# Kernel tuning notes

Measured on AMD Instinct MI355X. Metric: run time of the kernel, lower is better.

Reference implementation:

```python
import jax, jax.numpy as jnp
import numpy as np

NODES_PER_GRAPH = 40
NEG_SLOPE = 0.1


def gcn_conv(x, src, dst, deg_inv_sqrt, W, b):
    # PyG GCNConv: h = x @ W.T; symmetric-normalized aggregation with self-loops; + bias
    h = x @ W.T                                   # [N, out]
    norm = deg_inv_sqrt[src] * deg_inv_sqrt[dst]  # [E]
    msgs = h[src] * norm[:, None]                 # [E, out]
    agg = jax.ops.segment_sum(msgs, dst, num_segments=x.shape[0])
    # self-loop contribution: norm_ii = deg_inv_sqrt[i]^2 = 1/deg[i]
    agg = agg + h * (deg_inv_sqrt ** 2)[:, None]
    return agg + b


def setup_inputs() -> dict:
    key = jax.random.key(0)
    ks = jax.random.split(key, 12)
    N, E, C = 200000, 1000000, 40
    hid1, hid2, hid3, lin1, lin2, out = 128, 256, 128, 512, 128, 1

    def glorot(k, shape):
        fan_in = shape[-1]
        return jax.random.normal(k, shape, dtype=jnp.float32) * (1.0 / np.sqrt(fan_in))

    x = jax.random.normal(ks[0], (N, C), dtype=jnp.float32)
    edge_index = jax.random.randint(ks[1], (2, E), 0, N, dtype=jnp.int64)
    return {
        "x": x,
        "edge_index": edge_index,
        "W1": glorot(ks[2], (hid1, C)), "b1": jnp.zeros((hid1,), jnp.float32),
        "W2": glorot(ks[3], (hid2, hid1)), "b2": jnp.zeros((hid2,), jnp.float32),
        "W3": glorot(ks[4], (hid3, hid2)), "b3": jnp.zeros((hid3,), jnp.float32),
        "L1w": glorot(ks[5], (lin1, NODES_PER_GRAPH * hid3)), "L1b": jnp.zeros((lin1,), jnp.float32),
        "L2w": glorot(ks[6], (lin2, lin1)), "L2b": jnp.zeros((lin2,), jnp.float32),
        "L3w": glorot(ks[7], (out, lin2)), "L3b": jnp.zeros((out,), jnp.float32),
    }


def reference(x, edge_index, W1, b1, W2, b2, W3, b3, L1w, L1b, L2w, L2b, L3w, L3b):
    N = x.shape[0]
    src, dst = edge_index[0], edge_index[1]
    # degree with self-loops (edge weight 1), shared by all three convs
    deg = jax.ops.segment_sum(jnp.ones_like(dst, dtype=x.dtype), dst, num_segments=N) + 1.0
    deg_inv_sqrt = jax.lax.rsqrt(deg)

    lrelu = lambda v: jax.nn.leaky_relu(v, NEG_SLOPE)

    h = lrelu(gcn_conv(x, src, dst, deg_inv_sqrt, W1, b1))
    # dropout is identity in eval mode
    h = lrelu(gcn_conv(h, src, dst, deg_inv_sqrt, W2, b2))
    h = lrelu(gcn_conv(h, src, dst, deg_inv_sqrt, W3, b3))

    g = h.reshape(N // NODES_PER_GRAPH, -1)   # [G, 40*hid3]
    g = lrelu(g @ L1w.T + L1b)
    g = lrelu(g @ L2w.T + L2b)
    g = g @ L3w.T + L3b
    return jax.nn.sigmoid(g)                   # [G, 1]
```

## Files before the change

kernel.cpp:

```cpp
#include <hip/hip_runtime.h>
#include <cmath>

#define CDIV(a,b) (((a)+(b)-1)/(b))

typedef unsigned short bf16_t;
using short8 = __attribute__((ext_vector_type(8))) short;
using f32x4  = __attribute__((ext_vector_type(4))) float;
using u16x4  = __attribute__((ext_vector_type(4))) unsigned short;
using u16x8  = __attribute__((ext_vector_type(8))) unsigned short;

__device__ __forceinline__ float bf2f(unsigned short b) {
    unsigned u = ((unsigned)b) << 16;
    float f;
    __builtin_memcpy(&f, &u, 4);
    return f;
}
__device__ __forceinline__ unsigned short f2bf(float f) {
    unsigned u;
    __builtin_memcpy(&u, &f, 4);
    u = (u + 0x7FFFu + ((u >> 16) & 1u)) >> 16;
    return (unsigned short)u;
}

__device__ __forceinline__ void gload16(const bf16_t* g, unsigned short* l) {
    __builtin_amdgcn_global_load_lds(
        (const __attribute__((address_space(1))) void*)(g),
        (__attribute__((address_space(3))) void*)(l), 16, 0, 0);
}

__device__ __forceinline__ int edge_src(const int* ei, int E, int f, int i) {
    return f ? ei[2 * (size_t)i] : ei[i];
}
__device__ __forceinline__ int edge_dst(const int* ei, int E, int f, int i) {
    return f ? ei[2 * ((size_t)E + (size_t)i)] : ei[(size_t)E + (size_t)i];
}

__global__ __launch_bounds__(256) void k_packhist(const int* __restrict__ ei, int E,
                                                  int* __restrict__ src32,
                                                  int* __restrict__ dst32,
                                                  int* __restrict__ cnt8, int N) {
    __shared__ int sflag;
    int t = threadIdx.x;
    if (t < 64) {
        unsigned v = (unsigned)ei[2 * t + 1];
        unsigned long long m = __ballot(v != 0u);
        if (t == 0) sflag = (m == 0ULL) ? 1 : 0;
    }
    __syncthreads();
    int i = blockIdx.x * 256 + t;
    if (i >= E) return;
    int f = sflag;
    int s = edge_src(ei, E, f, i);
    int d = edge_dst(ei, E, f, i);
    src32[i] = s;
    dst32[i] = d;
    if ((unsigned)d < (unsigned)N)
        atomicAdd(&cnt8[(blockIdx.x & 7) * N + d], 1);
}

__global__ void k_blockred(const int* __restrict__ cnt8, int* __restrict__ bsum, int N) {
    __shared__ int sd[256];
    int b = blockIdx.x, t = threadIdx.x;
    int base = b * 1024 + t * 4;
    int s = 0;
#pragma unroll
    for (int i = 0; i < 4; i++) {
        int idx = base + i;
        if (idx < N)
#pragma unroll
            for (int r = 0; r < 8; r++) s += cnt8[r * N + idx];
    }
    sd[t] = s; __syncthreads();
    for (int off = 128; off > 0; off >>= 1) { if (t < off) sd[t] += sd[t + off]; __syncthreads(); }
    if (t == 0) bsum[b] = sd[0];
}

__global__ void k_scanwrite(const int* __restrict__ cnt8, const int* __restrict__ bsum,
                            int* __restrict__ rowptr, int* __restrict__ cur,
                            float* __restrict__ dis, int N, int nb) {
    __shared__ int sb[256];
    __shared__ int sd[256];
    int b = blockIdx.x, t = threadIdx.x;
    int v0 = (t < nb) ? bsum[t] : 0;
    sb[t] = v0; __syncthreads();
    for (int off = 1; off < 256; off <<= 1) {
        int y = (t >= off) ? sb[t - off] : 0;
        __syncthreads();
        sb[t] += y;
        __syncthreads();
    }
    int block_pre = (b == 0) ? 0 : sb[b - 1];

    int base = b * 1024 + t * 4;
    int tot[4]; int s = 0;
#pragma unroll
    for (int i = 0; i < 4; i++) {
        int idx = base + i;
        tot[i] = 0;
        if (idx < N) {
#pragma unroll
            for (int r = 0; r < 8; r++) tot[i] += cnt8[r * N + idx];
        }
        s += tot[i];
    }
    sd[t] = s; __syncthreads();
    for (int off = 1; off < 256; off <<= 1) {
        int y = (t >= off) ? sd[t - off] : 0;
        __syncthreads();
        sd[t] += y;
        __syncthreads();
    }
    int pre = block_pre + sd[t] - s;
#pragma unroll
    for (int i = 0; i < 4; i++) {
        int idx = base + i;
        if (idx < N) {
            rowptr[idx] = pre;
            cur[idx] = pre;
            dis[idx] = rsqrtf((float)tot[i] + 1.0f);
            pre += tot[i];
        } else if (idx == N) {
            rowptr[N] = pre;
        }
    }
}

#define FILL_EPB 4096
__global__ __launch_bounds__(256) void k_fill_r(
        const int* __restrict__ src32, const int* __restrict__ dst32, int E,
        int* __restrict__ cur, int* __restrict__ csr, int N, int NR) {
    int r = blockIdx.x & 7;
    int chunk = blockIdx.x >> 3;
    int lo = r * NR;
    int hi = min(lo + NR, N);
    int base = chunk * FILL_EPB;
    int end = min(base + FILL_EPB, E);
    for (int i = base + threadIdx.x; i < end; i += 256) {
        int d = dst32[i];
        if (d >= lo && d < hi) {
            int s = src32[i];
            if ((unsigned)s < (unsigned)N) {
                int p = atomicAdd(&cur[d], 1);
                csr[p] = s;
            }
        }
    }
}


struct WcSeg { const float* src; bf16_t* dst; int M, KW, KP, nchunk; };

__global__ __launch_bounds__(256) void k_wconv(WcSeg s0, WcSeg s1, WcSeg s2,
                                               WcSeg s3, WcSeg s4, WcSeg s5,
                                               int wtotal, int* __restrict__ zdst,
                                               int total) {
    int i = blockIdx.x * 256 + threadIdx.x;
    if (i >= total) return;
    if (i >= wtotal) {
        int4 z = {0, 0, 0, 0};
        *(int4*)(zdst + (size_t)(i - wtotal) * 4) = z;
        return;
    }
    WcSeg s;
    if (i < s0.nchunk) s = s0;
    else if ((i -= s0.nchunk) < s1.nchunk) s = s1;
    else if ((i -= s1.nchunk) < s2.nchunk) s = s2;
    else if ((i -= s2.nchunk) < s3.nchunk) s = s3;
    else if ((i -= s3.nchunk) < s4.nchunk) s = s4;
    else { i -= s4.nchunk; s = s5; }
    int cpr = s.KP >> 3;
    int row = i / cpr, kk = (i % cpr) << 3;
    short8 v = {};
    if (kk < s.KW) {
        const float4* p = (const float4*)(s.src + (size_t)row * s.KW + kk);
        float4 a = p[0], b = p[1];
        v[0] = (short)f2bf(a.x); v[1] = (short)f2bf(a.y);
        v[2] = (short)f2bf(a.z); v[3] = (short)f2bf(a.w);
        v[4] = (short)f2bf(b.x); v[5] = (short)f2bf(b.y);
        v[6] = (short)f2bf(b.z); v[7] = (short)f2bf(b.w);
    }
    *(short8*)(s.dst + (size_t)row * s.KP + kk) = v;
}


template <bool CBF, bool BIAS, int ACT, bool SPLIT>
__global__ __launch_bounds__(256) void gemm_mfma(
        const bf16_t* __restrict__ A, const bf16_t* __restrict__ Wb,
        const float* __restrict__ bias, void* __restrict__ Cv,
        int N, int K, int M, int Kseg, int nx, int ny) {
    constexpr int BM = 128, BK = 64;
    __shared__ __align__(16) unsigned short lds[4 * 64 * 68];
    unsigned short* Als = lds;
    unsigned short* Bls = lds + BM * BK;

    int t = threadIdx.x;
    int lane = t & 63, wid = t >> 6;
    int quad = lane >> 4, l15 = lane & 15;
    int wave_m = wid & 1, wave_n = wid >> 1;

    int bx, by, bz;
    if (SPLIT) {
        int bid = (int)blockIdx.x;
        int xcd = bid & 7, li = bid >> 3;
        bx = li % nx;
        int pl = li / nx;
        int ppx = (int)(gridDim.x >> 3) / nx;
        int pair = xcd * ppx + pl;
        by = pair % ny;
        bz = pair / ny;
    } else {
        bx = blockIdx.x; by = blockIdx.y; bz = 0;
    }

    int bm0 = by * BM;
    int bn0 = bx * BM;
    int kbeg = SPLIT ? bz * Kseg : 0;
    int kend = SPLIT ? min(kbeg + Kseg, K) : K;

    f32x4 acc[4][4] = {};

    for (int k0 = kbeg; k0 < kend; k0 += BK) {
#pragma unroll
        for (int it = 0; it < 4; it++) {
            int idx = t + it * 256;
            int row = idx >> 3, sc = idx & 7;
            int c = sc ^ (row & 7);
            int ga = bm0 + row; if (ga >= N) ga = N - 1;
            gload16(A + (size_t)ga * K + k0 + c * 8, Als + idx * 8);
            gload16(Wb + (size_t)(bn0 + row) * K + k0 + c * 8, Bls + idx * 8);
        }
        __syncthreads();

#pragma unroll
        for (int ks = 0; ks < 2; ks++) {
            short8 af[4], bfr[4];
            int ck = ks * 4 + quad;
            int sw = (ck ^ (l15 & 7)) << 3;
#pragma unroll
            for (int mt = 0; mt < 4; mt++)
                af[mt] = *(const short8*)&Als[(wave_m * 64 + mt * 16 + l15) * BK + sw];
#pragma unroll
            for (int nt = 0; nt < 4; nt++)
                bfr[nt] = *(const short8*)&Bls[(wave_n * 64 + nt * 16 + l15) * BK + sw];
#pragma unroll
            for (int mt = 0; mt < 4; mt++)
#pragma unroll
                for (int nt = 0; nt < 4; nt++)
                    acc[mt][nt] = __builtin_amdgcn_mfma_f32_16x16x32_bf16(
                        af[mt], bfr[nt], acc[mt][nt], 0, 0, 0);
        }
        __syncthreads();
    }

    if (!SPLIT && CBF) {
        constexpr int TST = 68;
        unsigned short* tw = lds + wid * 64 * TST;
#pragma unroll
        for (int mt = 0; mt < 4; mt++) {
#pragma unroll
            for (int nt = 0; nt < 4; nt++) {
                int tcol = nt * 16 + l15;
                float bv = BIAS ? bias[bn0 + wave_n * 64 + tcol] : 0.f;
#pragma unroll
                for (int r = 0; r < 4; r++) {
                    float x = acc[mt][nt][r];
                    if (BIAS) x += bv;
                    if (ACT == 1) x = x > 0.f ? x : 0.1f * x;
                    tw[(mt * 16 + quad * 4 + r) * TST + tcol] = f2bf(x);
                }
            }
        }
        __syncthreads();
        bf16_t* C = (bf16_t*)Cv;
        int lrow0 = lane >> 3, lcol = (lane & 7) * 8;
#pragma unroll
        for (int it = 0; it < 8; it++) {
            int lrow = it * 8 + lrow0;
            int row = bm0 + wave_m * 64 + lrow;
            if (row < N) {
                u16x8 v = *(const u16x8*)&tw[lrow * TST + lcol];
                *(u16x8*)&C[(size_t)row * M + bn0 + wave_n * 64 + lcol] = v;
            }
        }
    } else {
        float* Pz = SPLIT ? ((float*)Cv + (size_t)bz * N * M) : (float*)Cv;
#pragma unroll
        for (int mt = 0; mt < 4; mt++) {
            int rbase = bm0 + wave_m * 64 + mt * 16 + quad * 4;
#pragma unroll
            for (int nt = 0; nt < 4; nt++) {
                int col = bn0 + wave_n * 64 + nt * 16 + l15;
                float bv = (BIAS && !SPLIT) ? bias[col] : 0.f;
#pragma unroll
                for (int r = 0; r < 4; r++) {
                    int row = rbase + r;
                    if (row >= N) continue;
                    float x = acc[mt][nt][r];
                    if (!SPLIT) {
                        if (BIAS) x += bv;
                        if (ACT == 1) x = x > 0.f ? x : 0.1f * x;
                    }
                    Pz[(size_t)row * M + col] = x;
                }
            }
        }
    }
}

__global__ __launch_bounds__(256) void gemm_mlp2(
        const float* __restrict__ part6,
        const float* __restrict__ L1b,
        const bf16_t* __restrict__ Wb,
        float* __restrict__ Pout,
        int G) {
    constexpr int BM = 128, BK = 64, K = 512, M = 128, NY = 40;
    __shared__ __align__(16) unsigned short lds[2 * BM * BK];
    unsigned short* Als = lds;
    unsigned short* Bls = lds + BM * BK;

    int t = threadIdx.x;
    int lane = t & 63, wid = t >> 6;
    int quad = lane >> 4, l15 = lane & 15;
    int wave_m = wid & 1, wave_n = wid >> 1;

    int bid = (int)blockIdx.x;
    int xcd = bid & 7, li = bid >> 3;
    int ppx = (int)(gridDim.x >> 3);
    int pair = xcd * ppx + li;
    int by = pair % NY;
    int bz = pair / NY;

    int bm0 = by * BM;
    int kbeg = bz * (K / 4);
    size_t GK = (size_t)G * K;

    f32x4 acc[4][4] = {};

    for (int k0 = kbeg; k0 < kbeg + K / 4; k0 += BK) {
#pragma unroll
        for (int it = 0; it < 4; it++) {
            int idx = t + it * 256;
            int row = idx >> 3, sc = idx & 7;
            int cW = sc ^ (row & 7);
            gload16(Wb + (size_t)row * K + k0 + cW * 8, Bls + idx * 8);
            int g = bm0 + row; if (g >= G) g = G - 1;
            const float* pb = part6 + (size_t)g * K + k0 + sc * 8;
            float v[8] = {};
#pragma unroll
            for (int z = 0; z < 6; z++) {
                const float* pz = pb + (size_t)z * GK;
                float4 a = *(const float4*)pz;
                float4 b = *(const float4*)(pz + 4);
                v[0] += a.x; v[1] += a.y; v[2] += a.z; v[3] += a.w;
                v[4] += b.x; v[5] += b.y; v[6] += b.z; v[7] += b.w;
            }
            float4 b0 = *(const float4*)&L1b[k0 + sc * 8];
            float4 b1 = *(const float4*)&L1b[k0 + sc * 8 + 4];
            float bb[8] = {b0.x, b0.y, b0.z, b0.w, b1.x, b1.y, b1.z, b1.w};
            u16x8 o;
#pragma unroll
            for (int j = 0; j < 8; j++) {
                float xv = v[j] + bb[j];
                xv = xv > 0.f ? xv : 0.1f * xv;
                o[j] = f2bf(xv);
            }
            *(u16x8*)&Als[row * BK + ((sc ^ (row & 7)) << 3)] = o;
        }
        __syncthreads();

#pragma unroll
        for (int ks = 0; ks < 2; ks++) {
            short8 af[4], bfr[4];
            int ck = ks * 4 + quad;
            int sw = (ck ^ (l15 & 7)) << 3;
#pragma unroll
            for (int mt = 0; mt < 4; mt++)
                af[mt] = *(const short8*)&Als[(wave_m * 64 + mt * 16 + l15) * BK + sw];
#pragma unroll
            for (int nt = 0; nt < 4; nt++)
                bfr[nt] = *(const short8*)&Bls[(wave_n * 64 + nt * 16 + l15) * BK + sw];
#pragma unroll
            for (int mt = 0; mt < 4; mt++)
#pragma unroll
                for (int nt = 0; nt < 4; nt++)
                    acc[mt][nt] = __builtin_amdgcn_mfma_f32_16x16x32_bf16(
                        af[mt], bfr[nt], acc[mt][nt], 0, 0, 0);
        }
        __syncthreads();
    }

    float* Pz = Pout + (size_t)bz * G * M;
#pragma unroll
    for (int mt = 0; mt < 4; mt++) {
        int rbase = bm0 + wave_m * 64 + mt * 16 + quad * 4;
#pragma unroll
        for (int nt = 0; nt < 4; nt++) {
            int col = wave_n * 64 + nt * 16 + l15;
#pragma unroll
            for (int r = 0; r < 4; r++) {
                int row = rbase + r;
                if (row >= G) continue;
                Pz[(size_t)row * M + col] = acc[mt][nt][r];
            }
        }
    }
}

__global__ __launch_bounds__(256, 3) void gemm_fused23(
        const bf16_t* __restrict__ A,
        const bf16_t* __restrict__ W2,
        const float*  __restrict__ b2,
        const bf16_t* __restrict__ W3,
        bf16_t* __restrict__ C,
        int N) {
    __shared__ __align__(16) unsigned short lds[24576];
    unsigned short* Als  = lds;
    unsigned short* Bls  = lds + 4096;
    unsigned short* H2ls = lds;
    unsigned short* B2ls = lds + 16384;

    int t = threadIdx.x;
    int lane = t & 63, wid = t >> 6;
    int quad = lane >> 4, l15 = lane & 15;
    int wm = wid & 1, wn = wid >> 1;
    int bm0 = blockIdx.x * 64;

    float bv[8];
#pragma unroll
    for (int nt = 0; nt < 8; nt++) bv[nt] = b2[wn * 128 + nt * 16 + l15];

    f32x4 acc1[2][8] = {};
    for (int k0 = 0; k0 < 128; k0 += 64) {
#pragma unroll
        for (int it = 0; it < 2; it++) {
            int idx = t + it * 256;
            int row = idx >> 3, sc = idx & 7;
            int c = sc ^ (row & 7);
            int g = bm0 + row; if (g >= N) g = N - 1;
            gload16(A + (size_t)g * 128 + k0 + c * 8, Als + idx * 8);
        }
#pragma unroll
        for (int it = 0; it < 8; it++) {
            int idx = t + it * 256;
            int row = idx >> 3, sc = idx & 7;
            int c = sc ^ (row & 7);
            gload16(W2 + (size_t)row * 128 + k0 + c * 8, Bls + idx * 8);
        }
        __syncthreads();
#pragma unroll
        for (int ks = 0; ks < 2; ks++) {
            int ck = ks * 4 + quad;
            int sw = (ck ^ (l15 & 7)) << 3;
            short8 af[2];
#pragma unroll
            for (int mt = 0; mt < 2; mt++)
                af[mt] = *(const short8*)&Als[(wm * 32 + mt * 16 + l15) * 64 + sw];
#pragma unroll
            for (int nt = 0; nt < 8; nt++) {
                short8 bfr = *(const short8*)&Bls[(wn * 128 + nt * 16 + l15) * 64 + sw];
#pragma unroll
                for (int mt = 0; mt < 2; mt++)
                    acc1[mt][nt] = __builtin_amdgcn_mfma_f32_16x16x32_bf16(
                        af[mt], bfr, acc1[mt][nt], 0, 0, 0);
            }
        }
        __syncthreads();
    }

#pragma unroll
    for (int it = 0; it < 4; it++) {
        int idx = t + it * 256;
        int row = idx >> 3, sc = idx & 7;
        int c = sc ^ (row & 7);
        gload16(W3 + (size_t)row * 256 + c * 8, B2ls + idx * 8);
    }

#pragma unroll
    for (int mt = 0; mt < 2; mt++) {
#pragma unroll
        for (int nt = 0; nt < 8; nt++) {
            int col = wn * 128 + nt * 16 + l15;
            int chunk = col >> 3, within = col & 7;
#pragma unroll
            for (int r = 0; r < 4; r++) {
                int row = wm * 32 + mt * 16 + quad * 4 + r;
                float xv = acc1[mt][nt][r] + bv[nt];
                xv = xv > 0.f ? xv : 0.1f * xv;
                H2ls[row * 256 + ((chunk ^ (row & 7)) << 3) + within] = f2bf(xv);
            }
        }
    }
    __syncthreads();

    f32x4 acc2[2][4] = {};
    for (int k0 = 0; k0 < 256; k0 += 64) {
        if (k0 > 0) {
#pragma unroll
            for (int it = 0; it < 4; it++) {
                int idx = t + it * 256;
                int row = idx >> 3, sc = idx & 7;
                int c = sc ^ (row & 7);
                gload16(W3 + (size_t)row * 256 + k0 + c * 8, B2ls + idx * 8);
            }
            __syncthreads();
        }
#pragma unroll
        for (int ks = 0; ks < 2; ks++) {
            int kc = (k0 >> 3) + ks * 4 + quad;
            int swa = (kc ^ (l15 & 7)) << 3;
            int swb = ((ks * 4 + quad) ^ (l15 & 7)) << 3;
            short8 af[2], bfr[4];
#pragma unroll
            for (int mt = 0; mt < 2; mt++)
                af[mt] = *(const short8*)&H2ls[(wm * 32 + mt * 16 + l15) * 256 + swa];
#pragma unroll
            for (int nt = 0; nt < 4; nt++)
                bfr[nt] = *(const short8*)&B2ls[(wn * 64 + nt * 16 + l15) * 64 + swb];
#pragma unroll
            for (int mt = 0; mt < 2; mt++)
#pragma unroll
                for (int nt = 0; nt < 4; nt++)
                    acc2[mt][nt] = __builtin_amdgcn_mfma_f32_16x16x32_bf16(
                        af[mt], bfr[nt], acc2[mt][nt], 0, 0, 0);
        }
        __syncthreads();
    }

    constexpr int TST = 68;
    unsigned short* tw = lds + wid * 32 * TST;
#pragma unroll
    for (int mt = 0; mt < 2; mt++) {
#pragma unroll
        for (int nt = 0; nt < 4; nt++) {
            int tcol = nt * 16 + l15;
#pragma unroll
            for (int r = 0; r < 4; r++)
                tw[(mt * 16 + quad * 4 + r) * TST + tcol] = f2bf(acc2[mt][nt][r]);
        }
    }
    __syncthreads();
    int lrow0 = lane >> 3, lcol = (lane & 7) * 8;
#pragma unroll
    for (int it = 0; it < 4; it++) {
        int lrow = it * 8 + lrow0;
        int row = bm0 + wm * 32 + lrow;
        if (row < N) {
            u16x8 v = *(const u16x8*)&tw[lrow * TST + lcol];
            *(u16x8*)&C[(size_t)row * 128 + wn * 64 + lcol] = v;
        }
    }
}


template <int F, bool BACT>
__global__ __launch_bounds__(256) void k_agg(
        const bf16_t* __restrict__ H, const int* __restrict__ rowptr,
        const int* __restrict__ csr, const float* __restrict__ dis,
        const float* __restrict__ bias, bf16_t* __restrict__ out, int N) {
    constexpr int SUB = F / 8;
    constexpr int NPW = 64 / SUB;
    constexpr int SH  = (SUB == 16) ? 4 : 3;
    int gtid = blockIdx.x * 256 + threadIdx.x;
    int wave = gtid >> 6, lane = gtid & 63;
    int sub = lane >> SH, sl = lane & (SUB - 1);
    int node = wave * NPW + sub;
    if (node >= N) return;
    float di = dis[node];
    int s = rowptr[node], e = rowptr[node + 1];

    auto load_row = [&](const bf16_t* p, float (&r)[8]) {
        u16x8 v = *(const u16x8*)p;
#pragma unroll
        for (int f = 0; f < 8; f++) r[f] = bf2f(v[f]);
    };

    float acc[8], acc2[8];
    {
        float r[8];
        load_row(H + (size_t)node * F + sl * 8, r);
        float sln = di * di;
#pragma unroll
        for (int f = 0; f < 8; f++) { acc[f] = r[f] * sln; acc2[f] = 0.f; }
    }
    int p = s;
    for (; p + 4 <= e; p += 4) {
        int s0 = csr[p], s1 = csr[p + 1], s2 = csr[p + 2], s3 = csr[p + 3];
        float n0 = dis[s0] * di, n1 = dis[s1] * di;
        float n2 = dis[s2] * di, n3 = dis[s3] * di;
        float r0[8], r1[8], r2[8], r3[8];
        load_row(H + (size_t)s0 * F + sl * 8, r0);
        load_row(H + (size_t)s1 * F + sl * 8, r1);
        load_row(H + (size_t)s2 * F + sl * 8, r2);
        load_row(H + (size_t)s3 * F + sl * 8, r3);
#pragma unroll
        for (int f = 0; f < 8; f++) {
            acc[f]  += r0[f] * n0; acc2[f] += r1[f] * n1;
            acc[f]  += r2[f] * n2; acc2[f] += r3[f] * n3;
        }
    }
    if (p + 2 <= e) {
        int s0 = csr[p], s1 = csr[p + 1];
        float n0 = dis[s0] * di, n1 = dis[s1] * di;
        float r0[8], r1[8];
        load_row(H + (size_t)s0 * F + sl * 8, r0);
        load_row(H + (size_t)s1 * F + sl * 8, r1);
#pragma unroll
        for (int f = 0; f < 8; f++) { acc[f] += r0[f] * n0; acc2[f] += r1[f] * n1; }
        p += 2;
    }
    if (p < e) {
        int s0 = csr[p];
        float n0 = dis[s0] * di;
        float r0[8];
        load_row(H + (size_t)s0 * F + sl * 8, r0);
#pragma unroll
        for (int f = 0; f < 8; f++) acc[f] += r0[f] * n0;
    }

    float o[8];
#pragma unroll
    for (int f = 0; f < 8; f++) {
        float v = acc[f] + acc2[f];
        if (BACT) {
            v += bias[sl * 8 + f];
            v = v > 0.f ? v : 0.1f * v;
        }
        o[f] = v;
    }
    u16x8 w = {f2bf(o[0]), f2bf(o[1]), f2bf(o[2]), f2bf(o[3]),
               f2bf(o[4]), f2bf(o[5]), f2bf(o[6]), f2bf(o[7])};
    *(u16x8*)(out + (size_t)node * F + sl * 8) = w;
}


__global__ __launch_bounds__(256) void k_head2(
        const float* __restrict__ part, const float* __restrict__ L2b,
        const float* __restrict__ L3w, const float* __restrict__ L3b,
        float* __restrict__ out, int G) {
    int wv = (int)((blockIdx.x * blockDim.x + threadIdx.x) >> 6);
    int lane = threadIdx.x & 63;
    if (wv >= G) return;
    size_t base = (size_t)wv * 128 + lane * 2;
    size_t GM = (size_t)G * 128;
    float2 s = *(const float2*)&part[base];
#pragma unroll
    for (int z = 1; z < 4; z++) {
        float2 p = *(const float2*)&part[z * GM + base];
        s.x += p.x; s.y += p.y;
    }
    float2 b = *(const float2*)&L2b[lane * 2];
    float vx = s.x + b.x, vy = s.y + b.y;
    vx = vx > 0.f ? vx : 0.1f * vx;
    vy = vy > 0.f ? vy : 0.1f * vy;
    float2 wl = *(const float2*)&L3w[lane * 2];
    float d = vx * wl.x + vy * wl.y;
    for (int off = 32; off > 0; off >>= 1) d += __shfl_xor(d, off, 64);
    if (lane == 0) out[wv] = 1.f / (1.f + expf(-(d + L3b[0])));
}


extern "C" void kernel_launch(void* const* d_in, const int* in_sizes, int n_in,
                              void* d_out, int out_size, void* d_ws, size_t ws_size,
                              hipStream_t stream) {
    const float* x   = (const float*)d_in[0];
    const int*   ei  = (const int*)d_in[1];
    const float* W1  = (const float*)d_in[2];  const float* b1  = (const float*)d_in[3];
    const float* W2  = (const float*)d_in[4];  const float* b2  = (const float*)d_in[5];
    const float* W3  = (const float*)d_in[6];  const float* b3  = (const float*)d_in[7];
    const float* L1w = (const float*)d_in[8];  const float* L1b = (const float*)d_in[9];
    const float* L2w = (const float*)d_in[10]; const float* L2b = (const float*)d_in[11];
    const float* L3w = (const float*)d_in[12]; const float* L3b = (const float*)d_in[13];
    float* out = (float*)d_out;

    const int C = 40;
    const int N = in_sizes[0] / C;
    const int E = in_sizes[1] / 2;
    const int G = N / 40;
    const int H1d = 128, H2d = 256, H3d = 128, M1 = 512, M2 = 128;
    const int K1 = 40 * H3d;

    char* wsb = (char*)d_ws;
    size_t off = 0;
    auto alloc = [&](size_t bytes) -> void* {
        void* p = wsb + off;
        off += (bytes + 255) & ~(size_t)255;
        return p;
    };
    int*    cnt8   = (int*)alloc(4 * 8 * (size_t)N);
    int*    rowptr = (int*)alloc(4 * (size_t)(N + 1));
    int*    cur    = (int*)alloc(4 * (size_t)N);
    int*    csr    = (int*)alloc(4 * (size_t)E);
    int*    bsum   = (int*)alloc(4 * 512);
    float*  dis    = (float*)alloc(4 * (size_t)N);
    bf16_t* Hb     = (bf16_t*)alloc(2 * (size_t)N * H2d);
    bf16_t* Xb     = (bf16_t*)alloc(2 * (size_t)N * H2d);
    bf16_t* W1b    = (bf16_t*)alloc(2 * (size_t)H1d * 64);
    bf16_t* W2b    = (bf16_t*)alloc(2 * (size_t)H2d * H1d);
    bf16_t* W3b    = (bf16_t*)alloc(2 * (size_t)H3d * H2d);
    bf16_t* L1wb   = (bf16_t*)alloc(2 * (size_t)M1 * K1);
    bf16_t* L2wb   = (bf16_t*)alloc(2 * (size_t)M2 * M1);
    if (off > ws_size) return;

    int* src32 = (int*)Xb;
    int* dst32 = src32 + E;
    bf16_t* xb   = Hb;
    bf16_t* A1b  = Xb;
    bf16_t* H1   = Hb;
    bf16_t* A2   = Xb;
    bf16_t* H3p  = Xb;
    bf16_t* X3   = Hb;
    float*  part = (float*)Xb;
    float*  part2 = part + 6 * (size_t)G * M1;

    WcSeg s0 = {W1,  W1b,  H1d, 40,  64,  H1d * 64 / 8};
    WcSeg s1 = {W2,  W2b,  H2d, H1d, H1d, H2d * H1d / 8};
    WcSeg s2 = {W3,  W3b,  H3d, H2d, H2d, H3d * H2d / 8};
    WcSeg s3 = {L1w, L1wb, M1,  K1,  K1,  M1 * K1 / 8};
    WcSeg s4 = {L2w, L2wb, M2,  M1,  M1,  M2 * M1 / 8};
    WcSeg s5 = {x,   xb,   N,   40,  64,  N * 64 / 8};
    int wtotal = s0.nchunk + s1.nchunk + s2.nchunk + s3.nchunk + s4.nchunk + s5.nchunk;
    int ztotal = wtotal + 2 * N;
    k_wconv<<<CDIV(ztotal, 256), 256, 0, stream>>>(s0, s1, s2, s3, s4, s5,
                                                   wtotal, cnt8, ztotal);

    k_packhist<<<CDIV(E, 256), 256, 0, stream>>>(ei, E, src32, dst32, cnt8, N);
    int nb = CDIV(N + 1, 1024);
    k_blockred<<<nb, 256, 0, stream>>>(cnt8, bsum, N);
    k_scanwrite<<<nb, 256, 0, stream>>>(cnt8, bsum, rowptr, cur, dis, N, nb);
    int NR = CDIV(N, 8);
    k_fill_r<<<8 * CDIV(E, FILL_EPB), 256, 0, stream>>>(src32, dst32, E, cur, csr, N, NR);

    const int NB = CDIV(N, 128);
    const int GB = CDIV(G, 128);

    k_agg<64, false><<<CDIV(N, 32), 256, 0, stream>>>(xb, rowptr, csr, dis, nullptr, A1b, N);
    gemm_mfma<true, true, 1, false><<<dim3(1, NB), 256, 0, stream>>>(A1b, W1b, b1, H1, N, 64, H1d, 0, 0, 0);
    k_agg<128, false><<<CDIV(N, 16), 256, 0, stream>>>(H1, rowptr, csr, dis, nullptr, A2, N);
    gemm_fused23<<<CDIV(N, 64), 256, 0, stream>>>(A2, W2b, b2, W3b, H3p, N);
    k_agg<128, true><<<CDIV(N, 16), 256, 0, stream>>>(H3p, rowptr, csr, dis, b3, X3, N);

    gemm_mfma<false, false, 0, true><<<960, 256, 0, stream>>>(X3, L1wb, nullptr, part, G, K1, M1, 896, 4, 40);
    gemm_mlp2<<<160, 256, 0, stream>>>(part, L1b, L2wb, part2, G);
    k_head2<<<CDIV(G, 4), 256, 0, stream>>>(part2, L2b, L3w, L3b, out, G);
}
```

Measured before the change: 480.4 us.

## Make fused conv2/conv3 GEMM persistent with W2/W3 resident in LDS

Converts gemm_fused23 into a persistent kernel launched with 256 blocks that loops over 64-row tiles. Both weight matrices, W2 and W3 (160 KB total), are loaded once into LDS per block, so they are no longer re-streamed from global memory for every tile. The cost is that each block uses 160 KB of LDS, which allows only one block (4 waves) per CU. There is also no overlap between loading the A tile and running the MFMAs, so latency hiding may suffer.

```diff
diff --git a/kernel.cpp b/kernel.cpp
--- a/kernel.cpp
+++ b/kernel.cpp
@@ -406,148 +406,143 @@
     }
 }
 
-__global__ __launch_bounds__(256, 3) void gemm_fused23(
+__global__ __launch_bounds__(256, 1) void gemm_fused23(
         const bf16_t* __restrict__ A,
         const bf16_t* __restrict__ W2,
         const float*  __restrict__ b2,
         const bf16_t* __restrict__ W3,
         bf16_t* __restrict__ C,
-        int N) {
-    __shared__ __align__(16) unsigned short lds[24576];
-    unsigned short* Als  = lds;
-    unsigned short* Bls  = lds + 4096;
-    unsigned short* H2ls = lds;
-    unsigned short* B2ls = lds + 16384;
+        int N, int ntiles) {
+    __shared__ __align__(16) unsigned short lds[81920];
+    unsigned short* W2ls = lds;
+    unsigned short* W3ls = lds + 32768;
+    unsigned short* SH   = lds + 65536;
 
     int t = threadIdx.x;
     int lane = t & 63, wid = t >> 6;
     int quad = lane >> 4, l15 = lane & 15;
     int wm = wid & 1, wn = wid >> 1;
-    int bm0 = blockIdx.x * 64;
+
+#pragma unroll
+    for (int it = 0; it < 16; it++) {
+        int idx = t + it * 256;
+        int h = idx >> 11, r = (idx >> 3) & 255, sc = idx & 7;
+        int c = sc ^ (r & 7);
+        gload16(W2 + (size_t)r * 128 + h * 64 + c * 8, W2ls + idx * 8);
+    }
+#pragma unroll
+    for (int it = 0; it < 16; it++) {
+        int idx = t + it * 256;
+        int q = idx >> 10, r = (idx >> 3) & 127, sc = idx & 7;
+        int c = sc ^ (r & 7);
+        gload16(W3 + (size_t)r * 256 + q * 64 + c * 8, W3ls + idx * 8);
+    }
 
     float bv[8];
 #pragma unroll
     for (int nt = 0; nt < 8; nt++) bv[nt] = b2[wn * 128 + nt * 16 + l15];
 
-    f32x4 acc1[2][8] = {};
-    for (int k0 = 0; k0 < 128; k0 += 64) {
-#pragma unroll
-        for (int it = 0; it < 2; it++) {
+    for (int tile = blockIdx.x; tile < ntiles; tile += gridDim.x) {
+        int bm0 = tile * 64;
+#pragma unroll
+        for (int it = 0; it < 4; it++) {
             int idx = t + it * 256;
-            int row = idx >> 3, sc = idx & 7;
-            int c = sc ^ (row & 7);
-            int g = bm0 + row; if (g >= N) g = N - 1;
-            gload16(A + (size_t)g * 128 + k0 + c * 8, Als + idx * 8);
-        }
-#pragma unroll
-        for (int it = 0; it < 8; it++) {
-            int idx = t + it * 256;
-            int row = idx >> 3, sc = idx & 7;
-            int c = sc ^ (row & 7);
-            gload16(W2 + (size_t)row * 128 + k0 + c * 8, Bls + idx * 8);
-        }
-        __syncthreads();
-#pragma unroll
-        for (int ks = 0; ks < 2; ks++) {
-            int ck = ks * 4 + quad;
-            int sw = (ck ^ (l15 & 7)) << 3;
-            short8 af[2];
-#pragma unroll
-            for (int mt = 0; mt < 2; mt++)
-                af[mt] = *(const short8*)&Als[(wm * 32 + mt * 16 + l15) * 64 + sw];
+            int h = idx >> 9, r = (idx >> 3) & 63, sc = idx & 7;
+            int c = sc ^ (r & 7);
+            int g = bm0 + r; if (g >= N) g = N - 1;
+            gload16(A + (size_t)g * 128 + h * 64 + c * 8, SH + idx * 8);
+        }
+        __syncthreads();
+
+        f32x4 acc1[2][8] = {};
+#pragma unroll
+        for (int h = 0; h < 2; h++) {
+#pragma unroll
+            for (int ks = 0; ks < 2; ks++) {
+                int ck = ks * 4 + quad;
+                int sw = (ck ^ (l15 & 7)) << 3;
+                short8 af[2];
+#pragma unroll
+                for (int mt = 0; mt < 2; mt++)
+                    af[mt] = *(const short8*)&SH[(h * 64 + wm * 32 + mt * 16 + l15) * 64 + sw];
+#pragma unroll
+                for (int nt = 0; nt < 8; nt++) {
+                    short8 bfr = *(const short8*)&W2ls[(h * 256 + wn * 128 + nt * 16 + l15) * 64 + sw];
+#pragma unroll
+                    for (int mt = 0; mt < 2; mt++)
+                        acc1[mt][nt] = __builtin_amdgcn_mfma_f32_16x16x32_bf16(
+                            af[mt], bfr, acc1[mt][nt], 0, 0, 0);
+                }
+            }
+        }
+        __syncthreads();
+
+#pragma unroll
+        for (int mt = 0; mt < 2; mt++) {
 #pragma unroll
             for (int nt = 0; nt < 8; nt++) {
-                short8 bfr = *(const short8*)&Bls[(wn * 128 + nt * 16 + l15) * 64 + sw];
+                int col = wn * 128 + nt * 16 + l15;
+                int chunk = col >> 3, within = col & 7;
+#pragma unroll
+                for (int r = 0; r < 4; r++) {
+                    int row = wm * 32 + mt * 16 + quad * 4 + r;
+                    float xv = acc1[mt][nt][r] + bv[nt];
+                    xv = xv > 0.f ? xv : 0.1f * xv;
+                    SH[row * 256 + ((chunk ^ (row & 7)) << 3) + within] = f2bf(xv);
+                }
+            }
+        }
+        __syncthreads();
+
+        f32x4 acc2[2][4] = {};
+#pragma unroll
+        for (int q = 0; q < 4; q++) {
+#pragma unroll
+            for (int ks = 0; ks < 2; ks++) {
+                int kc = q * 8 + ks * 4 + quad;
+                int swa = (kc ^ (l15 & 7)) << 3;
+                int swb = ((ks * 4 + quad) ^ (l15 & 7)) << 3;
+                short8 af[2], bfr[4];
 #pragma unroll
                 for (int mt = 0; mt < 2; mt++)
-                    acc1[mt][nt] = __builtin_amdgcn_mfma_f32_16x16x32_bf16(
-                        af[mt], bfr, acc1[mt][nt], 0, 0, 0);
-            }
-        }
-        __syncthreads();
-    }
-
-#pragma unroll
-    for (int it = 0; it < 4; it++) {
-        int idx = t + it * 256;
-        int row = idx >> 3, sc = idx & 7;
-        int c = sc ^ (row & 7);
-        gload16(W3 + (size_t)row * 256 + c * 8, B2ls + idx * 8);
-    }
-
-#pragma unroll
-    for (int mt = 0; mt < 2; mt++) {
-#pragma unroll
-        for (int nt = 0; nt < 8; nt++) {
-            int col = wn * 128 + nt * 16 + l15;
-            int chunk = col >> 3, within = col & 7;
-#pragma unroll
-            for (int r = 0; r < 4; r++) {
-                int row = wm * 32 + mt * 16 + quad * 4 + r;
-                float xv = acc1[mt][nt][r] + bv[nt];
-                xv = xv > 0.f ? xv : 0.1f * xv;
-                H2ls[row * 256 + ((chunk ^ (row & 7)) << 3) + within] = f2bf(xv);
-            }
-        }
-    }
-    __syncthreads();
-
-    f32x4 acc2[2][4] = {};
-    for (int k0 = 0; k0 < 256; k0 += 64) {
-        if (k0 > 0) {
-#pragma unroll
-            for (int it = 0; it < 4; it++) {
-                int idx = t + it * 256;
-                int row = idx >> 3, sc = idx & 7;
-                int c = sc ^ (row & 7);
-                gload16(W3 + (size_t)row * 256 + k0 + c * 8, B2ls + idx * 8);
-            }
-            __syncthreads();
-        }
-#pragma unroll
-        for (int ks = 0; ks < 2; ks++) {
-            int kc = (k0 >> 3) + ks * 4 + quad;
-            int swa = (kc ^ (l15 & 7)) << 3;
-            int swb = ((ks * 4 + quad) ^ (l15 & 7)) << 3;
-            short8 af[2], bfr[4];
-#pragma unroll
-            for (int mt = 0; mt < 2; mt++)
-                af[mt] = *(const short8*)&H2ls[(wm * 32 + mt * 16 + l15) * 256 + swa];
-#pragma unroll
-            for (int nt = 0; nt < 4; nt++)
-                bfr[nt] = *(const short8*)&B2ls[(wn * 64 + nt * 16 + l15) * 64 + swb];
-#pragma unroll
-            for (int mt = 0; mt < 2; mt++)
+                    af[mt] = *(const short8*)&SH[(wm * 32 + mt * 16 + l15) * 256 + swa];
 #pragma unroll
                 for (int nt = 0; nt < 4; nt++)
-                    acc2[mt][nt] = __builtin_amdgcn_mfma_f32_16x16x32_bf16(
-                        af[mt], bfr[nt], acc2[mt][nt], 0, 0, 0);
-        }
-        __syncthreads();
-    }
-
-    constexpr int TST = 68;
-    unsigned short* tw = lds + wid * 32 * TST;
-#pragma unroll
-    for (int mt = 0; mt < 2; mt++) {
-#pragma unroll
-        for (int nt = 0; nt < 4; nt++) {
-            int tcol = nt * 16 + l15;
-#pragma unroll
-            for (int r = 0; r < 4; r++)
-                tw[(mt * 16 + quad * 4 + r) * TST + tcol] = f2bf(acc2[mt][nt][r]);
-        }
-    }
-    __syncthreads();
-    int lrow0 = lane >> 3, lcol = (lane & 7) * 8;
-#pragma unroll
-    for (int it = 0; it < 4; it++) {
-        int lrow = it * 8 + lrow0;
-        int row = bm0 + wm * 32 + lrow;
-        if (row < N) {
-            u16x8 v = *(const u16x8*)&tw[lrow * TST + lcol];
-            *(u16x8*)&C[(size_t)row * 128 + wn * 64 + lcol] = v;
-        }
+                    bfr[nt] = *(const short8*)&W3ls[(q * 128 + wn * 64 + nt * 16 + l15) * 64 + swb];
+#pragma unroll
+                for (int mt = 0; mt < 2; mt++)
+#pragma unroll
+                    for (int nt = 0; nt < 4; nt++)
+                        acc2[mt][nt] = __builtin_amdgcn_mfma_f32_16x16x32_bf16(
+                            af[mt], bfr[nt], acc2[mt][nt], 0, 0, 0);
+            }
+        }
+        __syncthreads();
+
+        constexpr int TST = 68;
+        unsigned short* tw = SH + wid * 32 * TST;
+#pragma unroll
+        for (int mt = 0; mt < 2; mt++) {
+#pragma unroll
+            for (int nt = 0; nt < 4; nt++) {
+                int tcol = nt * 16 + l15;
+#pragma unroll
+                for (int r = 0; r < 4; r++)
+                    tw[(mt * 16 + quad * 4 + r) * TST + tcol] = f2bf(acc2[mt][nt][r]);
+            }
+        }
+        __syncthreads();
+        int lrow0 = lane >> 3, lcol = (lane & 7) * 8;
+#pragma unroll
+        for (int it = 0; it < 4; it++) {
+            int lrow = it * 8 + lrow0;
+            int row = bm0 + wm * 32 + lrow;
+            if (row < N) {
+                u16x8 v = *(const u16x8*)&tw[lrow * TST + lcol];
+                *(u16x8*)&C[(size_t)row * 128 + wn * 64 + lcol] = v;
+            }
+        }
+        __syncthreads();
     }
 }
 
@@ -736,7 +731,7 @@
     k_agg<64, false><<<CDIV(N, 32), 256, 0, stream>>>(xb, rowptr, csr, dis, nullptr, A1b, N);
     gemm_mfma<true, true, 1, false><<<dim3(1, NB), 256, 0, stream>>>(A1b, W1b, b1, H1, N, 64, H1d, 0, 0, 0);
     k_agg<128, false><<<CDIV(N, 16), 256, 0, stream>>>(H1, rowptr, csr, dis, nullptr, A2, N);
-    gemm_fused23<<<CDIV(N, 64), 256, 0, stream>>>(A2, W2b, b2, W3b, H3p, N);
+    gemm_fused23<<<256, 256, 0, stream>>>(A2, W2b, b2, W3b, H3p, N, CDIV(N, 64));
     k_agg<128, true><<<CDIV(N, 16), 256, 0, stream>>>(H3p, rowptr, csr, dis, b3, X3, N);
 
     gemm_mfma<false, false, 0, true><<<960, 256, 0, stream>>>(X3, L1wb, nullptr, part, G, K1, M1, 896, 4, 40);
```

New measurement: 491.1 us. 1.02x slower.
